# Kernel optimization log

Measured on AMD Instinct MI355X. Metric: run time of the kernel, lower is better.

## Reference

```python
import jax, jax.numpy as jnp
import numpy as np

INP_DIM, OUT_DIM, MID_DIM, MID_LAYERS = 3, 1, 4, 2


def _uniform(key, shape, bound):
    return jax.random.uniform(key, shape, jnp.float32, -bound, bound)


def setup_inputs() -> dict:
    key = jax.random.key(0)
    ks = jax.random.split(key, 16)
    B, T = 4096, 1024
    bnd = 1.0 / np.sqrt(MID_DIM)  # PyTorch LSTM/Linear init bound
    d = {
        "x": jax.random.normal(ks[0], (B, T, INP_DIM), jnp.float32),
        # layer 0 LSTM (gate order i,f,g,o stacked along rows)
        "W_ih0": _uniform(ks[1], (4 * MID_DIM, INP_DIM), bnd),
        "W_hh0": _uniform(ks[2], (4 * MID_DIM, MID_DIM), bnd),
        "b_ih0": _uniform(ks[3], (4 * MID_DIM,), bnd),
        "b_hh0": _uniform(ks[4], (4 * MID_DIM,), bnd),
        # layer 1 LSTM
        "W_ih1": _uniform(ks[5], (4 * MID_DIM, MID_DIM), bnd),
        "W_hh1": _uniform(ks[6], (4 * MID_DIM, MID_DIM), bnd),
        "b_ih1": _uniform(ks[7], (4 * MID_DIM,), bnd),
        "b_hh1": _uniform(ks[8], (4 * MID_DIM,), bnd),
        "W1": _uniform(ks[9], (MID_DIM, MID_DIM), bnd),
        "b1": _uniform(ks[10], (MID_DIM,), bnd),
        "W2": _uniform(ks[11], (OUT_DIM, MID_DIM), bnd),
        "b2": _uniform(ks[12], (OUT_DIM,), bnd),
    }
    return d


def _lstm_layer(x_tbd, W_ih, W_hh, b_ih, b_hh):
    # x_tbd: [T, B, D] time-major. Precompute input contribution to all gates.
    H = W_hh.shape[1]
    xg = jnp.einsum("tbd,gd->tbg", x_tbd, W_ih) + (b_ih + b_hh)  # [T,B,4H]

    def step(carry, xg_t):
        h, c = carry
        g = xg_t + h @ W_hh.T  # [B,4H]
        i, f, gg, o = jnp.split(g, 4, axis=-1)
        i = jax.nn.sigmoid(i)
        f = jax.nn.sigmoid(f)
        gg = jnp.tanh(gg)
        o = jax.nn.sigmoid(o)
        c = f * c + i * gg
        h = o * jnp.tanh(c)
        return (h, c), h

    B = x_tbd.shape[1]
    init = (jnp.zeros((B, H), x_tbd.dtype), jnp.zeros((B, H), x_tbd.dtype))
    _, hs = jax.lax.scan(step, init, xg)
    return hs  # [T,B,H]


def reference(x, W_ih0, W_hh0, b_ih0, b_hh0, W_ih1, W_hh1, b_ih1, b_hh1, W1, b1, W2, b2):
    # x: [B,T,3] (batch_first). Run 2-layer LSTM then per-timestep MLP head.
    h = jnp.transpose(x, (1, 0, 2))  # -> [T,B,3]
    h = _lstm_layer(h, W_ih0, W_hh0, b_ih0, b_hh0)
    h = _lstm_layer(h, W_ih1, W_hh1, b_ih1, b_hh1)
    h = jnp.transpose(h, (1, 0, 2))  # -> [B,T,H]
    y = jnp.tanh(h @ W1.T + b1) @ W2.T + b2  # [B,T,1]
    return y
```

## Files before the change

kernel.cpp:

```cpp
#include <hip/hip_runtime.h>


#define T_STEPS 1024
#define BATCH   4096
#define CHUNK   16
#define NCHUNK  (T_STEPS / CHUNK)
#define RDEPTH  4

__device__ __forceinline__ float fast_exp2(float x) {
#if __has_builtin(__builtin_amdgcn_exp2f)
    return __builtin_amdgcn_exp2f(x);
#else
    return exp2f(x);
#endif
}

__device__ __forceinline__ float fast_rcp(float x) {
#if __has_builtin(__builtin_amdgcn_rcpf)
    return __builtin_amdgcn_rcpf(x);
#else
    return 1.0f / x;
#endif
}

__device__ __forceinline__ float fast_tanh(float x) {
    return 2.0f * fast_rcp(1.0f + fast_exp2(-2.88539008f * x)) - 1.0f;
}

template <int CTRL>
__device__ __forceinline__ float dpp_mov(float v) {
    int i = __builtin_bit_cast(int, v);
    i = __builtin_amdgcn_mov_dpp(i, CTRL, 0xF, 0xF, true);
    return __builtin_bit_cast(float, i);
}

#define DPP_QB0         0x00
#define DPP_QB1         0x55
#define DPP_QB2         0xAA
#define DPP_QB3         0xFF
#define DPP_ROR8        0x128
#define DPP_MIRROR      0x140
#define DPP_HALF_MIRROR 0x141
#define DPP_QSWAP2      0x4E
#define DPP_QSWAP1      0xB1

__global__ __launch_bounds__(768) void lstm_r9_kernel(
    const float* __restrict__ x,
    const float* __restrict__ W_ih0, const float* __restrict__ W_hh0,
    const float* __restrict__ b_ih0, const float* __restrict__ b_hh0,
    const float* __restrict__ W_ih1, const float* __restrict__ W_hh1,
    const float* __restrict__ b_ih1, const float* __restrict__ b_hh1,
    const float* __restrict__ W1, const float* __restrict__ b1,
    const float* __restrict__ W2, const float* __restrict__ b2,
    float* __restrict__ out)
{
    __shared__ float4 xstage[4][2][68];
    __shared__ float4 ring0[4][RDEPTH][CHUNK][4];
    __shared__ float4 ring1[4][RDEPTH][CHUNK][4];
    __shared__ int done0[4][RDEPTH];
    __shared__ int free0[4][RDEPTH];
    __shared__ int done1[4][RDEPTH];
    __shared__ int free1[4][RDEPTH];

    const int tid  = threadIdx.x;
    const int wave = tid >> 6;
    const int stg  = wave >> 2;
    const int pr   = wave & 3;
    const int lane = tid & 63;
    const int idx  = lane & 15;
    const int rho  = lane & 3;
    const int u    = (lane >> 2) & 3;
    const int r    = rho * 4 + u;
    const int ch   = lane >> 4;
    const int batch = blockIdx.x * 16 + pr * 4 + ch;

    if (tid < 4 * RDEPTH) {
        done0[tid >> 2][tid & 3] = 0;
        free0[tid >> 2][tid & 3] = 0;
        done1[tid >> 2][tid & 3] = 0;
        free1[tid >> 2][tid & 3] = 0;
    }
    __syncthreads();

    const float am = (rho == 2) ? -2.88539008f : -1.44269504f;
    const float aa = (rho == 2) ? 2.0f : 1.0f;
    const float ab = (rho == 2) ? -1.0f : 0.0f;

    if (stg == 0) {
        const float wx0 = W_ih0[r * 3 + 0];
        const float wx1 = W_ih0[r * 3 + 1];
        const float wx2 = W_ih0[r * 3 + 2];
        const float bias0 = b_ih0[r] + b_hh0[r];
        float wh0[4];
#pragma unroll
        for (int k = 0; k < 4; ++k) wh0[k] = W_hh0[r * 4 + (u ^ k)];

        float h0 = 0.f, c0 = 0.f, h0b = 0.f, h0c = 0.f, h0d = 0.f;

        const float* xrow = x + (size_t)batch * T_STEPS * 3;
        const float* p0 = xrow + idx * 3;
        xstage[pr][0][ch * 17 + idx] = make_float4(p0[0], p0[1], p0[2], 0.f);
        const float* p1 = xrow + 48 + idx * 3;
        float q0 = p1[0], q1 = p1[1], q2 = p1[2];

        volatile int* ff = &free0[pr][0];

        for (int c = 0; c < NCHUNK; ++c) {
            const int s = c & (RDEPTH - 1);
            if (c >= RDEPTH) {
                while (ff[s] < c - RDEPTH + 1) { __builtin_amdgcn_s_sleep(1); }
            }

            const float4* xs = &xstage[pr][c & 1][ch * 17];
            float4 xc = xs[0];
#pragma unroll
            for (int tt = 0; tt < CHUNK; ++tt) {
                float4 xn = xs[(tt < CHUNK - 1) ? tt + 1 : tt];

                float pre0 = bias0 + wx0 * xc.x + wx1 * xc.y + wx2 * xc.z
                           + wh0[0] * h0 + wh0[1] * h0b + wh0[2] * h0c + wh0[3] * h0d;
                float a0 = aa * fast_rcp(1.0f + fast_exp2(am * pre0)) + ab;
                float gi = dpp_mov<DPP_QB0>(a0);
                float gf = dpp_mov<DPP_QB1>(a0);
                float gg = dpp_mov<DPP_QB2>(a0);
                float go = dpp_mov<DPP_QB3>(a0);
                c0 = gf * c0 + gi * gg;
                h0 = go * fast_tanh(c0);
                h0b = dpp_mov<DPP_HALF_MIRROR>(h0);
                h0c = dpp_mov<DPP_ROR8>(h0);
                h0d = dpp_mov<DPP_MIRROR>(h0);

                if (rho == 0) ((float*)&ring0[pr][s][tt][ch])[u] = h0;
                xc = xn;
            }
            __threadfence_block();
            if (lane == 0) done0[pr][s] = c + 1;

            if (c < NCHUNK - 1)
                xstage[pr][(c + 1) & 1][ch * 17 + idx] = make_float4(q0, q1, q2, 0.f);
            if (c < NCHUNK - 2) {
                const float* p = xrow + (c + 2) * 48 + idx * 3;
                q0 = p[0]; q1 = p[1]; q2 = p[2];
            }
        }
    } else if (stg == 1) {
        const float bias1 = b_ih1[r] + b_hh1[r];
        float wi1[4], wh1[4];
#pragma unroll
        for (int k = 0; k < 4; ++k) {
            wi1[k] = W_ih1[r * 4 + k];
            wh1[k] = W_hh1[r * 4 + (u ^ k)];
        }

        float h1 = 0.f, c1 = 0.f, h1b = 0.f, h1c = 0.f, h1d = 0.f;

        volatile int* df = &done0[pr][0];
        volatile int* f1 = &free1[pr][0];

        for (int c = 0; c < NCHUNK; ++c) {
            const int s = c & (RDEPTH - 1);
            while (df[s] < c + 1) { __builtin_amdgcn_s_sleep(1); }
            if (c >= RDEPTH) {
                while (f1[s] < c - RDEPTH + 1) { __builtin_amdgcn_s_sleep(1); }
            }
            __threadfence_block();

            const float4* rgp = &ring0[pr][s][0][ch];
            float4 h_a = rgp[0];
            float4 h_b = rgp[4];
#pragma unroll
            for (int tt = 0; tt < CHUNK; ++tt) {
                float4 h_n = rgp[4 * ((tt < CHUNK - 2) ? tt + 2 : CHUNK - 1)];

                float pre1 = bias1
                           + wi1[0] * h_a.x + wi1[1] * h_a.y
                           + wi1[2] * h_a.z + wi1[3] * h_a.w
                           + wh1[0] * h1 + wh1[1] * h1b + wh1[2] * h1c + wh1[3] * h1d;
                float a1 = aa * fast_rcp(1.0f + fast_exp2(am * pre1)) + ab;
                float gi1 = dpp_mov<DPP_QB0>(a1);
                float gf1 = dpp_mov<DPP_QB1>(a1);
                float gg1 = dpp_mov<DPP_QB2>(a1);
                float go1 = dpp_mov<DPP_QB3>(a1);
                c1 = gf1 * c1 + gi1 * gg1;
                h1 = go1 * fast_tanh(c1);
                h1b = dpp_mov<DPP_HALF_MIRROR>(h1);
                h1c = dpp_mov<DPP_ROR8>(h1);
                h1d = dpp_mov<DPP_MIRROR>(h1);

                if (rho == 0) ((float*)&ring1[pr][s][tt][ch])[u] = h1;

                h_a = h_b; h_b = h_n;
            }
            if (lane == 0) free0[pr][s] = c + 1;
            __threadfence_block();
            if (lane == 0) done1[pr][s] = c + 1;
        }
    } else {
        const int cu  = lane & 3;
        const int sb  = (lane >> 2) & 3;
        const int cch = lane >> 4;
        const int cbatch = blockIdx.x * 16 + pr * 4 + cch;

        float w1r[4];
#pragma unroll
        for (int k = 0; k < 4; ++k) w1r[k] = W1[cu * 4 + k];
        const float b1u = b1[cu];
        const float w2u = W2[cu];
        const float b2v = b2[0];
        float* op = out + (size_t)cbatch * T_STEPS;

        volatile int* d1 = &done1[pr][0];

        for (int c = 0; c < NCHUNK; ++c) {
            const int s = c & (RDEPTH - 1);
            while (d1[s] < c + 1) { __builtin_amdgcn_s_sleep(1); }
            __threadfence_block();

            const float4* rg = &ring1[pr][s][sb][cch];
            float yq[4];
#pragma unroll
            for (int it = 0; it < 4; ++it) {
                float4 h = rg[it * 16];
                float zp = b1u + w1r[0] * h.x + w1r[1] * h.y
                               + w1r[2] * h.z + w1r[3] * h.w;
                float z  = fast_tanh(zp);
                float yv = w2u * z;
                float t1 = yv + dpp_mov<DPP_QSWAP2>(yv);
                yq[it]   = t1 + dpp_mov<DPP_QSWAP1>(t1) + b2v;
            }
            if (lane == 0) free1[pr][s] = c + 1;

            if (cu == 0) {
#pragma unroll
                for (int it = 0; it < 4; ++it)
                    op[c * CHUNK + it * 4 + sb] = yq[it];
            }
        }
    }
}

extern "C" void kernel_launch(void* const* d_in, const int* in_sizes, int n_in,
                              void* d_out, int out_size, void* d_ws, size_t ws_size,
                              hipStream_t stream) {
    const float* x     = (const float*)d_in[0];
    const float* W_ih0 = (const float*)d_in[1];
    const float* W_hh0 = (const float*)d_in[2];
    const float* b_ih0 = (const float*)d_in[3];
    const float* b_hh0 = (const float*)d_in[4];
    const float* W_ih1 = (const float*)d_in[5];
    const float* W_hh1 = (const float*)d_in[6];
    const float* b_ih1 = (const float*)d_in[7];
    const float* b_hh1 = (const float*)d_in[8];
    const float* W1    = (const float*)d_in[9];
    const float* b1    = (const float*)d_in[10];
    const float* W2    = (const float*)d_in[11];
    const float* b2    = (const float*)d_in[12];
    float* out = (float*)d_out;

    dim3 grid(BATCH / 16);
    dim3 block(768);
    lstm_r9_kernel<<<grid, block, 0, stream>>>(
        x, W_ih0, W_hh0, b_ih0, b_hh0, W_ih1, W_hh1, b_ih1, b_hh1,
        W1, b1, W2, b2, out);
}
```

Baseline: 249.8 us.

## Interleave two batch groups per LSTM wave to hide recurrence latency

Each layer-0 and layer-1 wave now processes two independent batch groups with interleaved instruction streams, so the block drops from 12 to 8 waves (2+2+4). The independent chains let the scheduler overlap the transcendental and DPP latency of one recurrence with the other, and fewer waves per block may allow more blocks per CU. The cost is more registers per wave, and each wave now waits on the slower of two groups' ring flags, which couples their progress.

Result: slower. 291.2 us (+16.5%).

```diff
diff --git a/kernel.cpp b/kernel.cpp
--- a/kernel.cpp
+++ b/kernel.cpp
@@ -44,7 +44,7 @@
 #define DPP_QSWAP2      0x4E
 #define DPP_QSWAP1      0xB1
 
-__global__ __launch_bounds__(768) void lstm_r9_kernel(
+__global__ __launch_bounds__(512) void lstm_r10_kernel(
     const float* __restrict__ x,
     const float* __restrict__ W_ih0, const float* __restrict__ W_hh0,
     const float* __restrict__ b_ih0, const float* __restrict__ b_hh0,
@@ -64,15 +64,12 @@
 
     const int tid  = threadIdx.x;
     const int wave = tid >> 6;
-    const int stg  = wave >> 2;
-    const int pr   = wave & 3;
     const int lane = tid & 63;
     const int idx  = lane & 15;
     const int rho  = lane & 3;
     const int u    = (lane >> 2) & 3;
     const int r    = rho * 4 + u;
     const int ch   = lane >> 4;
-    const int batch = blockIdx.x * 16 + pr * 4 + ch;
 
     if (tid < 4 * RDEPTH) {
         done0[tid >> 2][tid & 3] = 0;
@@ -86,7 +83,8 @@
     const float aa = (rho == 2) ? 2.0f : 1.0f;
     const float ab = (rho == 2) ? -1.0f : 0.0f;
 
-    if (stg == 0) {
+    if (wave < 2) {
+        const int g0 = wave * 2, g1 = g0 + 1;
         const float wx0 = W_ih0[r * 3 + 0];
         const float wx1 = W_ih0[r * 3 + 1];
         const float wx2 = W_ih0[r * 3 + 2];
@@ -95,55 +93,90 @@
 #pragma unroll
         for (int k = 0; k < 4; ++k) wh0[k] = W_hh0[r * 4 + (u ^ k)];
 
-        float h0 = 0.f, c0 = 0.f, h0b = 0.f, h0c = 0.f, h0d = 0.f;
-
-        const float* xrow = x + (size_t)batch * T_STEPS * 3;
-        const float* p0 = xrow + idx * 3;
-        xstage[pr][0][ch * 17 + idx] = make_float4(p0[0], p0[1], p0[2], 0.f);
-        const float* p1 = xrow + 48 + idx * 3;
-        float q0 = p1[0], q1 = p1[1], q2 = p1[2];
-
-        volatile int* ff = &free0[pr][0];
+        float h0_0 = 0.f, c0_0 = 0.f, h0b_0 = 0.f, h0c_0 = 0.f, h0d_0 = 0.f;
+        float h0_1 = 0.f, c0_1 = 0.f, h0b_1 = 0.f, h0c_1 = 0.f, h0d_1 = 0.f;
+
+        const float* xrow0 = x + (size_t)(blockIdx.x * 16 + g0 * 4 + ch) * T_STEPS * 3;
+        const float* xrow1 = x + (size_t)(blockIdx.x * 16 + g1 * 4 + ch) * T_STEPS * 3;
+        {
+            const float* pa = xrow0 + idx * 3;
+            xstage[g0][0][ch * 17 + idx] = make_float4(pa[0], pa[1], pa[2], 0.f);
+            const float* pb = xrow1 + idx * 3;
+            xstage[g1][0][ch * 17 + idx] = make_float4(pb[0], pb[1], pb[2], 0.f);
+        }
+        const float* p1a = xrow0 + 48 + idx * 3;
+        float qa0 = p1a[0], qa1 = p1a[1], qa2 = p1a[2];
+        const float* p1b = xrow1 + 48 + idx * 3;
+        float qb0 = p1b[0], qb1 = p1b[1], qb2 = p1b[2];
+
+        volatile int* ff0 = &free0[g0][0];
+        volatile int* ff1 = &free0[g1][0];
 
         for (int c = 0; c < NCHUNK; ++c) {
             const int s = c & (RDEPTH - 1);
             if (c >= RDEPTH) {
-                while (ff[s] < c - RDEPTH + 1) { __builtin_amdgcn_s_sleep(1); }
-            }
-
-            const float4* xs = &xstage[pr][c & 1][ch * 17];
-            float4 xc = xs[0];
+                const int lim = c - RDEPTH + 1;
+                while (ff0[s] < lim || ff1[s] < lim) { __builtin_amdgcn_s_sleep(1); }
+            }
+
+            const float4* xs0 = &xstage[g0][c & 1][ch * 17];
+            const float4* xs1 = &xstage[g1][c & 1][ch * 17];
+            float4 xc0 = xs0[0];
+            float4 xc1 = xs1[0];
 #pragma unroll
             for (int tt = 0; tt < CHUNK; ++tt) {
-                float4 xn = xs[(tt < CHUNK - 1) ? tt + 1 : tt];
-
-                float pre0 = bias0 + wx0 * xc.x + wx1 * xc.y + wx2 * xc.z
-                           + wh0[0] * h0 + wh0[1] * h0b + wh0[2] * h0c + wh0[3] * h0d;
-                float a0 = aa * fast_rcp(1.0f + fast_exp2(am * pre0)) + ab;
-                float gi = dpp_mov<DPP_QB0>(a0);
-                float gf = dpp_mov<DPP_QB1>(a0);
-                float gg = dpp_mov<DPP_QB2>(a0);
-                float go = dpp_mov<DPP_QB3>(a0);
-                c0 = gf * c0 + gi * gg;
-                h0 = go * fast_tanh(c0);
-                h0b = dpp_mov<DPP_HALF_MIRROR>(h0);
-                h0c = dpp_mov<DPP_ROR8>(h0);
-                h0d = dpp_mov<DPP_MIRROR>(h0);
-
-                if (rho == 0) ((float*)&ring0[pr][s][tt][ch])[u] = h0;
-                xc = xn;
+                const int nx = (tt < CHUNK - 1) ? tt + 1 : tt;
+                float4 xn0 = xs0[nx];
+                float4 xn1 = xs1[nx];
+
+                float pre_0 = bias0 + wx0 * xc0.x + wx1 * xc0.y + wx2 * xc0.z
+                            + wh0[0] * h0_0 + wh0[1] * h0b_0 + wh0[2] * h0c_0 + wh0[3] * h0d_0;
+                float pre_1 = bias0 + wx0 * xc1.x + wx1 * xc1.y + wx2 * xc1.z
+                            + wh0[0] * h0_1 + wh0[1] * h0b_1 + wh0[2] * h0c_1 + wh0[3] * h0d_1;
+                float a_0 = aa * fast_rcp(1.0f + fast_exp2(am * pre_0)) + ab;
+                float a_1 = aa * fast_rcp(1.0f + fast_exp2(am * pre_1)) + ab;
+                float gi0 = dpp_mov<DPP_QB0>(a_0);
+                float gf0 = dpp_mov<DPP_QB1>(a_0);
+                float gg0 = dpp_mov<DPP_QB2>(a_0);
+                float go0 = dpp_mov<DPP_QB3>(a_0);
+                float gi1 = dpp_mov<DPP_QB0>(a_1);
+                float gf1 = dpp_mov<DPP_QB1>(a_1);
+                float gg1 = dpp_mov<DPP_QB2>(a_1);
+                float go1 = dpp_mov<DPP_QB3>(a_1);
+                c0_0 = gf0 * c0_0 + gi0 * gg0;
+                c0_1 = gf1 * c0_1 + gi1 * gg1;
+                h0_0 = go0 * fast_tanh(c0_0);
+                h0_1 = go1 * fast_tanh(c0_1);
+                h0b_0 = dpp_mov<DPP_HALF_MIRROR>(h0_0);
+                h0c_0 = dpp_mov<DPP_ROR8>(h0_0);
+                h0d_0 = dpp_mov<DPP_MIRROR>(h0_0);
+                h0b_1 = dpp_mov<DPP_HALF_MIRROR>(h0_1);
+                h0c_1 = dpp_mov<DPP_ROR8>(h0_1);
+                h0d_1 = dpp_mov<DPP_MIRROR>(h0_1);
+
+                if (rho == 0) {
+                    ((float*)&ring0[g0][s][tt][ch])[u] = h0_0;
+                    ((float*)&ring0[g1][s][tt][ch])[u] = h0_1;
+                }
+                xc0 = xn0;
+                xc1 = xn1;
             }
             __threadfence_block();
-            if (lane == 0) done0[pr][s] = c + 1;
-
-            if (c < NCHUNK - 1)
-                xstage[pr][(c + 1) & 1][ch * 17 + idx] = make_float4(q0, q1, q2, 0.f);
+            if (lane == 0) { done0[g0][s] = c + 1; done0[g1][s] = c + 1; }
+
+            if (c < NCHUNK - 1) {
+                xstage[g0][(c + 1) & 1][ch * 17 + idx] = make_float4(qa0, qa1, qa2, 0.f);
+                xstage[g1][(c + 1) & 1][ch * 17 + idx] = make_float4(qb0, qb1, qb2, 0.f);
+            }
             if (c < NCHUNK - 2) {
-                const float* p = xrow + (c + 2) * 48 + idx * 3;
-                q0 = p[0]; q1 = p[1]; q2 = p[2];
-            }
-        }
-    } else if (stg == 1) {
+                const float* pa = xrow0 + (c + 2) * 48 + idx * 3;
+                qa0 = pa[0]; qa1 = pa[1]; qa2 = pa[2];
+                const float* pb = xrow1 + (c + 2) * 48 + idx * 3;
+                qb0 = pb[0]; qb1 = pb[1]; qb2 = pb[2];
+            }
+        }
+    } else if (wave < 4) {
+        const int g0 = (wave - 2) * 2, g1 = g0 + 1;
         const float bias1 = b_ih1[r] + b_hh1[r];
         float wi1[4], wh1[4];
 #pragma unroll
@@ -152,54 +185,82 @@
             wh1[k] = W_hh1[r * 4 + (u ^ k)];
         }
 
-        float h1 = 0.f, c1 = 0.f, h1b = 0.f, h1c = 0.f, h1d = 0.f;
-
-        volatile int* df = &done0[pr][0];
-        volatile int* f1 = &free1[pr][0];
+        float h1_0 = 0.f, c1_0 = 0.f, h1b_0 = 0.f, h1c_0 = 0.f, h1d_0 = 0.f;
+        float h1_1 = 0.f, c1_1 = 0.f, h1b_1 = 0.f, h1c_1 = 0.f, h1d_1 = 0.f;
+
+        volatile int* df0 = &done0[g0][0];
+        volatile int* df1 = &done0[g1][0];
+        volatile int* f10 = &free1[g0][0];
+        volatile int* f11 = &free1[g1][0];
 
         for (int c = 0; c < NCHUNK; ++c) {
             const int s = c & (RDEPTH - 1);
-            while (df[s] < c + 1) { __builtin_amdgcn_s_sleep(1); }
+            while (df0[s] < c + 1 || df1[s] < c + 1) { __builtin_amdgcn_s_sleep(1); }
             if (c >= RDEPTH) {
-                while (f1[s] < c - RDEPTH + 1) { __builtin_amdgcn_s_sleep(1); }
+                const int lim = c - RDEPTH + 1;
+                while (f10[s] < lim || f11[s] < lim) { __builtin_amdgcn_s_sleep(1); }
             }
             __threadfence_block();
 
-            const float4* rgp = &ring0[pr][s][0][ch];
-            float4 h_a = rgp[0];
-            float4 h_b = rgp[4];
+            const float4* rg0 = &ring0[g0][s][0][ch];
+            const float4* rg1 = &ring0[g1][s][0][ch];
+            float4 ha0 = rg0[0];
+            float4 hb0 = rg0[4];
+            float4 ha1 = rg1[0];
+            float4 hb1 = rg1[4];
 #pragma unroll
             for (int tt = 0; tt < CHUNK; ++tt) {
-                float4 h_n = rgp[4 * ((tt < CHUNK - 2) ? tt + 2 : CHUNK - 1)];
-
-                float pre1 = bias1
-                           + wi1[0] * h_a.x + wi1[1] * h_a.y
-                           + wi1[2] * h_a.z + wi1[3] * h_a.w
-                           + wh1[0] * h1 + wh1[1] * h1b + wh1[2] * h1c + wh1[3] * h1d;
-                float a1 = aa * fast_rcp(1.0f + fast_exp2(am * pre1)) + ab;
-                float gi1 = dpp_mov<DPP_QB0>(a1);
-                float gf1 = dpp_mov<DPP_QB1>(a1);
-                float gg1 = dpp_mov<DPP_QB2>(a1);
-                float go1 = dpp_mov<DPP_QB3>(a1);
-                c1 = gf1 * c1 + gi1 * gg1;
-                h1 = go1 * fast_tanh(c1);
-                h1b = dpp_mov<DPP_HALF_MIRROR>(h1);
-                h1c = dpp_mov<DPP_ROR8>(h1);
-                h1d = dpp_mov<DPP_MIRROR>(h1);
-
-                if (rho == 0) ((float*)&ring1[pr][s][tt][ch])[u] = h1;
-
-                h_a = h_b; h_b = h_n;
-            }
-            if (lane == 0) free0[pr][s] = c + 1;
+                const int nf = 4 * ((tt < CHUNK - 2) ? tt + 2 : CHUNK - 1);
+                float4 hn0 = rg0[nf];
+                float4 hn1 = rg1[nf];
+
+                float pre_0 = bias1
+                            + wi1[0] * ha0.x + wi1[1] * ha0.y
+                            + wi1[2] * ha0.z + wi1[3] * ha0.w
+                            + wh1[0] * h1_0 + wh1[1] * h1b_0 + wh1[2] * h1c_0 + wh1[3] * h1d_0;
+                float pre_1 = bias1
+                            + wi1[0] * ha1.x + wi1[1] * ha1.y
+                            + wi1[2] * ha1.z + wi1[3] * ha1.w
+                            + wh1[0] * h1_1 + wh1[1] * h1b_1 + wh1[2] * h1c_1 + wh1[3] * h1d_1;
+                float a_0 = aa * fast_rcp(1.0f + fast_exp2(am * pre_0)) + ab;
+                float a_1 = aa * fast_rcp(1.0f + fast_exp2(am * pre_1)) + ab;
+                float gi0 = dpp_mov<DPP_QB0>(a_0);
+                float gf0 = dpp_mov<DPP_QB1>(a_0);
+                float gg0 = dpp_mov<DPP_QB2>(a_0);
+                float go0 = dpp_mov<DPP_QB3>(a_0);
+                float gi1 = dpp_mov<DPP_QB0>(a_1);
+                float gf1 = dpp_mov<DPP_QB1>(a_1);
+                float gg1 = dpp_mov<DPP_QB2>(a_1);
+                float go1 = dpp_mov<DPP_QB3>(a_1);
+                c1_0 = gf0 * c1_0 + gi0 * gg0;
+                c1_1 = gf1 * c1_1 + gi1 * gg1;
+                h1_0 = go0 * fast_tanh(c1_0);
+                h1_1 = go1 * fast_tanh(c1_1);
+                h1b_0 = dpp_mov<DPP_HALF_MIRROR>(h1_0);
+                h1c_0 = dpp_mov<DPP_ROR8>(h1_0);
+                h1d_0 = dpp_mov<DPP_MIRROR>(h1_0);
+                h1b_1 = dpp_mov<DPP_HALF_MIRROR>(h1_1);
+                h1c_1 = dpp_mov<DPP_ROR8>(h1_1);
+                h1d_1 = dpp_mov<DPP_MIRROR>(h1_1);
+
+                if (rho == 0) {
+                    ((float*)&ring1[g0][s][tt][ch])[u] = h1_0;
+                    ((float*)&ring1[g1][s][tt][ch])[u] = h1_1;
+                }
+
+                ha0 = hb0; hb0 = hn0;
+                ha1 = hb1; hb1 = hn1;
+            }
+            if (lane == 0) { free0[g0][s] = c + 1; free0[g1][s] = c + 1; }
             __threadfence_block();
-            if (lane == 0) done1[pr][s] = c + 1;
+            if (lane == 0) { done1[g0][s] = c + 1; done1[g1][s] = c + 1; }
         }
     } else {
+        const int grp = wave - 4;
         const int cu  = lane & 3;
         const int sb  = (lane >> 2) & 3;
         const int cch = lane >> 4;
-        const int cbatch = blockIdx.x * 16 + pr * 4 + cch;
+        const int cbatch = blockIdx.x * 16 + grp * 4 + cch;
 
         float w1r[4];
 #pragma unroll
@@ -209,14 +270,14 @@
         const float b2v = b2[0];
         float* op = out + (size_t)cbatch * T_STEPS;
 
-        volatile int* d1 = &done1[pr][0];
+        volatile int* d1 = &done1[grp][0];
 
         for (int c = 0; c < NCHUNK; ++c) {
             const int s = c & (RDEPTH - 1);
             while (d1[s] < c + 1) { __builtin_amdgcn_s_sleep(1); }
             __threadfence_block();
 
-            const float4* rg = &ring1[pr][s][sb][cch];
+            const float4* rg = &ring1[grp][s][sb][cch];
             float yq[4];
 #pragma unroll
             for (int it = 0; it < 4; ++it) {
@@ -228,7 +289,7 @@
                 float t1 = yv + dpp_mov<DPP_QSWAP2>(yv);
                 yq[it]   = t1 + dpp_mov<DPP_QSWAP1>(t1) + b2v;
             }
-            if (lane == 0) free1[pr][s] = c + 1;
+            if (lane == 0) free1[grp][s] = c + 1;
 
             if (cu == 0) {
 #pragma unroll
@@ -258,8 +319,8 @@
     float* out = (float*)d_out;
 
     dim3 grid(BATCH / 16);
-    dim3 block(768);
-    lstm_r9_kernel<<<grid, block, 0, stream>>>(
+    dim3 block(512);
+    lstm_r10_kernel<<<grid, block, 0, stream>>>(
         x, W_ih0, W_hh0, b_ih0, b_hh0, W_ih1, W_hh1, b_ih1, b_hh1,
         W1, b1, W2, b2, out);
 }
```
